# Optimization experiments

Measured on AMD Instinct MI355X. Metric: run time of the kernel, lower is better.

## Reference

```python
import jax, jax.numpy as jnp
import numpy as np

B = 1
N_HEADS = 8
SEQ = 4096
HEAD_DIM = 128
BLOCK = 64          # sparse_block_size == kernel_block_size
LOCAL_BLOCKS = 16
VERT_STRIDE = 8


def _token_mask():
    """Local + vertical-strided block-sparse causal mask, per head.

    Block (qb, kb) is active for head h iff qb >= kb and
    (qb - kb < LOCAL_BLOCKS  or  (kb + h*head_step + 1) % VERT_STRIDE == 0),
    then expanded to token level and AND-ed with the token causal mask.
    """
    nb = SEQ // BLOCK
    qb = jnp.arange(nb)[:, None]                      # [nb, 1]
    kb = jnp.arange(nb)[None, :]                      # [1, nb]
    head_step = max(1, VERT_STRIDE // N_HEADS)        # hetero heads (homo_head=False)
    h = jnp.arange(N_HEADS)[:, None, None]            # [H, 1, 1]
    vert = (kb[None] + h * head_step + 1) % VERT_STRIDE == 0   # [H, 1, nb] -> broadcast
    local = (qb - kb >= 0) & (qb - kb < LOCAL_BLOCKS)          # [nb, nb]
    bmask = (qb >= kb)[None] & (local[None] | vert)            # [H, nb, nb]
    # expand block mask to token level
    tmask = jnp.repeat(jnp.repeat(bmask, BLOCK, axis=1), BLOCK, axis=2)  # [H, S, S]
    causal = jnp.arange(SEQ)[:, None] >= jnp.arange(SEQ)[None, :]
    return tmask & causal[None]


def setup_inputs() -> dict:
    key = jax.random.key(0)
    kq, kk, kv = jax.random.split(key, 3)
    q = jax.random.normal(kq, (B, N_HEADS, SEQ, HEAD_DIM), jnp.float32)
    k = jax.random.normal(kk, (B, N_HEADS, SEQ, HEAD_DIM), jnp.float32)
    v = jax.random.normal(kv, (B, N_HEADS, SEQ, HEAD_DIM), jnp.float32)
    sm_scale = jnp.float32(1.0 / np.sqrt(HEAD_DIM))
    return {"q": q, "k": k, "v": v, "sm_scale": sm_scale}


def reference(q, k, v, sm_scale):
    mask = _token_mask()                                       # [H, S, S] bool
    scores = jnp.einsum('bhqd,bhkd->bhqk', q, k) * sm_scale    # [B, H, S, S]
    neg = jnp.asarray(jnp.finfo(scores.dtype).min, scores.dtype)
    scores = jnp.where(mask[None], scores, neg)
    p = jax.nn.softmax(scores, axis=-1)
    return jnp.einsum('bhqk,bhkd->bhqd', p, v)
```

## Files before the change

kernel.cpp:

```cpp
#include <hip/hip_runtime.h>
#include <hip/hip_bf16.h>

#define HH 8
#define SEQL 4096
#define DD 128
#define NBLK 64
#define LOCAL_B 16
#define MBIAS 12.0f
#define EP_STR 132

typedef __attribute__((ext_vector_type(8))) short bf16x8;
typedef __attribute__((ext_vector_type(4))) float f32x4;
typedef unsigned short ushort_t;

typedef const __attribute__((address_space(1))) unsigned int gu32;
typedef __attribute__((address_space(3))) unsigned int lu32;

__device__ __forceinline__ unsigned short f2bf(float x) {
    union { float f; unsigned u; } a; a.f = x;
    unsigned r = a.u + 0x7FFFu + ((a.u >> 16) & 1u);
    return (unsigned short)(r >> 16);
}

__device__ __forceinline__ unsigned cvtpk_bf16(float lo, float hi) {
    unsigned r;
    asm("v_cvt_pk_bf16_f32 %0, %1, %2" : "=v"(r) : "v"(lo), "v"(hi));
    return r;
}

__device__ __forceinline__ void gload16(const void* src, void* ldsdst) {
    __builtin_amdgcn_global_load_lds((gu32*)src, (lu32*)ldsdst, 16, 0, 0);
}

#define T_STR 136
__global__ void prep(const float* __restrict__ k, const float* __restrict__ v,
                     ushort_t* __restrict__ kb, ushort_t* __restrict__ vt) {
    __shared__ ushort_t t[64 * T_STR];
    int bid = blockIdx.x;
    int tid = threadIdx.x;
    if (bid < 2048) {
        int idx = (bid * 256 + tid) * 8;
        const float4* s = (const float4*)(k + idx);
        float4 a = s[0], b = s[1];
        union { bf16x8 v8; ushort_t u[8]; } p;
        p.u[0] = f2bf(a.x); p.u[1] = f2bf(a.y); p.u[2] = f2bf(a.z); p.u[3] = f2bf(a.w);
        p.u[4] = f2bf(b.x); p.u[5] = f2bf(b.y); p.u[6] = f2bf(b.z); p.u[7] = f2bf(b.w);
        *(bf16x8*)(kb + idx) = p.v8;
        return;
    }
    int g = bid - 2048;
    int h  = g >> 6;
    int sb = g & 63;
    const float* vp = v + ((size_t)h * SEQL + sb * 64) * DD;
    {
        int col = (tid & 15) * 8;
        #pragma unroll
        for (int it = 0; it < 4; ++it) {
            int row = it * 16 + (tid >> 4);
            const float4* s = (const float4*)(vp + row * DD + col);
            float4 a = s[0], b = s[1];
            union { bf16x8 v8; ushort_t u[8]; } p;
            p.u[0] = f2bf(a.x); p.u[1] = f2bf(a.y); p.u[2] = f2bf(a.z); p.u[3] = f2bf(a.w);
            p.u[4] = f2bf(b.x); p.u[5] = f2bf(b.y); p.u[6] = f2bf(b.z); p.u[7] = f2bf(b.w);
            *(bf16x8*)&t[row * T_STR + col] = p.v8;
        }
    }
    __syncthreads();
    {
        int d = tid >> 1, seg = tid & 1;
        ushort_t* dst = vt + ((size_t)h * DD + d) * SEQL + sb * 64 + seg * 32;
        #pragma unroll
        for (int i = 0; i < 4; ++i) {
            union { bf16x8 v8; ushort_t u[8]; } o;
            #pragma unroll
            for (int e = 0; e < 8; ++e)
                o.u[e] = t[(seg * 32 + i * 8 + e) * T_STR + d];
            *(bf16x8*)(dst + i * 8) = o.v8;
        }
    }
}

__global__ __launch_bounds__(256, 2)
void bsattn5(const float* __restrict__ q, const ushort_t* __restrict__ kbuf,
             const ushort_t* __restrict__ vtbuf, const float* __restrict__ scl,
             float* __restrict__ out) {
    const int g  = blockIdx.x;
    const int h  = g & 7;
    const int i0 = g >> 3;
    const int qb = (i0 < 32) ? (63 - i0) : (i0 - 32);
    const int tid = threadIdx.x;
    const int w  = tid >> 6;
    const int l  = tid & 63;
    const int lr = l & 15;
    const int lg = l >> 4;

    __shared__ char smem[65536];

    const float kappa = scl[0] * 1.44269504088896f;

    const float*    qh = q     + (size_t)h * SEQL * DD;
    const ushort_t* kh = kbuf  + (size_t)h * SEQL * DD;
    const ushort_t* vh = vtbuf + (size_t)h * DD * SEQL;
    float*          oh = out   + (size_t)h * SEQL * DD;

    bf16x8 qf[4];
    {
        const float* qrow = qh + (size_t)(qb * 64 + 16 * w + lr) * DD;
        #pragma unroll
        for (int ks = 0; ks < 4; ++ks) {
            const float4* p4 = (const float4*)(qrow + ks * 32 + lg * 8);
            float4 x = p4[0], y = p4[1];
            union { bf16x8 v8; ushort_t u[8]; } pk;
            pk.u[0] = f2bf(x.x * kappa); pk.u[1] = f2bf(x.y * kappa);
            pk.u[2] = f2bf(x.z * kappa); pk.u[3] = f2bf(x.w * kappa);
            pk.u[4] = f2bf(y.x * kappa); pk.u[5] = f2bf(y.y * kappa);
            pk.u[6] = f2bf(y.z * kappa); pk.u[7] = f2bf(y.w * kappa);
            qf[ks] = pk.v8;
        }
    }

    f32x4 oacc[8];
    #pragma unroll
    for (int i = 0; i < 8; ++i) oacc[i] = (f32x4){0.f, 0.f, 0.f, 0.f};
    float lrun = 0.f;

    unsigned swz = (unsigned)((lg * 16) ^ ((lr & 7) << 4));
    unsigned kA = (unsigned)(lr * 256) + swz;
    unsigned kB = kA ^ 64u;
    unsigned vA = 32768u + (unsigned)(lr * 128) + swz;
    unsigned vB = vA ^ 64u;
    unsigned kst = 0, vst = 0;

    auto stage = [&](int kb) {
        const char* kbase = (const char*)(kh + (size_t)kb * 64 * DD);
        char* kdst = smem + kst;
        #pragma unroll
        for (int j = 0; j < 4; ++j) {
            int row  = w * 16 + j * 4 + (l >> 4);
            int colb = ((l & 15) << 4) ^ ((row & 7) << 4);
            gload16(kbase + row * 256 + colb, kdst + (w * 16 + j * 4) * 256);
        }
        const char* vbase = (const char*)vh + (size_t)kb * 128;
        char* vdst = smem + 32768 + vst;
        #pragma unroll
        for (int j = 0; j < 4; ++j) {
            int d0 = w * 32 + j * 8;
            int d  = d0 + (l >> 3);
            int colb = ((l & 7) << 4) ^ ((d & 7) << 4);
            gload16(vbase + (size_t)d * (SEQL * 2) + colb, vdst + d0 * 128);
        }
        kst ^= 16384u; vst ^= 16384u;
    };

    const bool selA = (lg >= 2);
    const bool b1 = (lg & 1);
    const bool b2 = (lg & 2);

    auto compute = [&](bool diag) {
        f32x4 sacc[4];
        #pragma unroll
        for (int ct = 0; ct < 4; ++ct)
            sacc[ct] = (f32x4){-MBIAS, -MBIAS, -MBIAS, -MBIAS};
        __builtin_amdgcn_s_setprio(1);
        #pragma unroll
        for (int ks = 0; ks < 4; ++ks) {
            #pragma unroll
            for (int ct = 0; ct < 4; ++ct) {
                bf16x8 kf = *(const bf16x8*)(smem + ((ks & 1) ? kB : kA) +
                                             ct * 4096 + (ks >> 1) * 128);
                sacc[ct] = __builtin_amdgcn_mfma_f32_16x16x32_bf16(kf, qf[ks], sacc[ct], 0, 0, 0);
            }
        }
        __builtin_amdgcn_s_setprio(0);

        float p[4][4];
        #pragma unroll
        for (int ct = 0; ct < 4; ++ct)
            #pragma unroll
            for (int j = 0; j < 4; ++j)
                p[ct][j] = exp2f(sacc[ct][j]);
        if (diag) {
            #pragma unroll
            for (int ct = 0; ct < 4; ++ct)
                #pragma unroll
                for (int j = 0; j < 4; ++j)
                    if (16 * ct + 4 * lg + j > 16 * w + lr) p[ct][j] = 0.f;
        }
        float rs = 0.f;
        #pragma unroll
        for (int ct = 0; ct < 4; ++ct)
            #pragma unroll
            for (int j = 0; j < 4; ++j) rs += p[ct][j];
        lrun += rs;

        unsigned e0 = cvtpk_bf16(p[0][0], p[0][1]), e1 = cvtpk_bf16(p[0][2], p[0][3]);
        unsigned e2 = cvtpk_bf16(p[2][0], p[2][1]), e3 = cvtpk_bf16(p[2][2], p[2][3]);
        unsigned o0 = cvtpk_bf16(p[1][0], p[1][1]), o1 = cvtpk_bf16(p[1][2], p[1][3]);
        unsigned o2 = cvtpk_bf16(p[3][0], p[3][1]), o3 = cvtpk_bf16(p[3][2], p[3][3]);

        union { unsigned u[4]; bf16x8 v8; } pb0, pb1;
        {
            unsigned m = selA ? o0 : e0, n = selA ? e0 : o0;
            unsigned t  = __shfl_xor((int)n, 32);
            unsigned tp = __shfl_xor((int)n, 48);
            unsigned m16 = __shfl_xor((int)m, 16);
            pb0.u[0] = b1 ? (b2 ? m16 : tp) : (b2 ? t : m);
            pb0.u[2] = b1 ? (b2 ? m : t) : (b2 ? tp : m16);
        }
        {
            unsigned m = selA ? o1 : e1, n = selA ? e1 : o1;
            unsigned t  = __shfl_xor((int)n, 32);
            unsigned tp = __shfl_xor((int)n, 48);
            unsigned m16 = __shfl_xor((int)m, 16);
            pb0.u[1] = b1 ? (b2 ? m16 : tp) : (b2 ? t : m);
            pb0.u[3] = b1 ? (b2 ? m : t) : (b2 ? tp : m16);
        }
        {
            unsigned m = selA ? o2 : e2, n = selA ? e2 : o2;
            unsigned t  = __shfl_xor((int)n, 32);
            unsigned tp = __shfl_xor((int)n, 48);
            unsigned m16 = __shfl_xor((int)m, 16);
            pb1.u[0] = b1 ? (b2 ? m16 : tp) : (b2 ? t : m);
            pb1.u[2] = b1 ? (b2 ? m : t) : (b2 ? tp : m16);
        }
        {
            unsigned m = selA ? o3 : e3, n = selA ? e3 : o3;
            unsigned t  = __shfl_xor((int)n, 32);
            unsigned tp = __shfl_xor((int)n, 48);
            unsigned m16 = __shfl_xor((int)m, 16);
            pb1.u[1] = b1 ? (b2 ? m16 : tp) : (b2 ? t : m);
            pb1.u[3] = b1 ? (b2 ? m : t) : (b2 ? tp : m16);
        }

        __builtin_amdgcn_s_setprio(1);
        #pragma unroll
        for (int dt = 0; dt < 8; ++dt) {
            bf16x8 vf = *(const bf16x8*)(smem + vA + dt * 2048);
            oacc[dt] = __builtin_amdgcn_mfma_f32_16x16x32_bf16(vf, pb0.v8, oacc[dt], 0, 0, 0);
        }
        #pragma unroll
        for (int dt = 0; dt < 8; ++dt) {
            bf16x8 vf = *(const bf16x8*)(smem + vB + dt * 2048);
            oacc[dt] = __builtin_amdgcn_mfma_f32_16x16x32_bf16(vf, pb1.v8, oacc[dt], 0, 0, 0);
        }
        __builtin_amdgcn_s_setprio(0);
    };

    const int vstart = (7 - h) & 7;
    int lo = qb - (LOCAL_B - 1); if (lo < 0) lo = 0;
    int kb = (vstart <= qb - LOCAL_B) ? vstart : lo;
    stage(kb);
    for (;;) {
        int kn;
        if (kb < lo) { int n = kb + 8; kn = (n <= qb - LOCAL_B) ? n : lo; }
        else if (kb < qb) kn = kb + 1;
        else kn = -1;

        if (kn >= 0) {
            stage(kn);
            asm volatile("s_waitcnt vmcnt(8)" ::: "memory");
            __builtin_amdgcn_sched_barrier(0);
            __builtin_amdgcn_s_barrier();
            __builtin_amdgcn_sched_barrier(0);
            compute(false);
            __builtin_amdgcn_s_barrier();
            kA ^= 16384u; kB ^= 16384u; vA ^= 16384u; vB ^= 16384u;
            kb = kn;
        } else {
            asm volatile("s_waitcnt vmcnt(0)" ::: "memory");
            __builtin_amdgcn_sched_barrier(0);
            __builtin_amdgcn_s_barrier();
            __builtin_amdgcn_sched_barrier(0);
            compute(true);
            __builtin_amdgcn_s_barrier();
            break;
        }
    }

    float tot = lrun;
    tot += __shfl_xor(tot, 16);
    tot += __shfl_xor(tot, 32);
    float rcp = 1.0f / tot;

    float* ep  = (float*)smem;
    float* epw = ep + w * 16 * EP_STR;
    #pragma unroll
    for (int dt = 0; dt < 8; ++dt)
        #pragma unroll
        for (int j = 0; j < 4; ++j)
            epw[lr * EP_STR + dt * 16 + 4 * lg + j] = oacc[dt][j] * rcp;
    __syncthreads();
    {
        int qr  = tid >> 2;
        int seg = tid & 3;
        const float* rp = ep + (qr >> 4) * (16 * EP_STR) + (qr & 15) * EP_STR + seg * 32;
        float* op = oh + (size_t)(qb * 64 + qr) * DD + seg * 32;
        #pragma unroll
        for (int i = 0; i < 8; ++i)
            ((float4*)op)[i] = ((const float4*)rp)[i];
    }
}

extern "C" void kernel_launch(void* const* d_in, const int* in_sizes, int n_in,
                              void* d_out, int out_size, void* d_ws, size_t ws_size,
                              hipStream_t stream) {
    const float* q   = (const float*)d_in[0];
    const float* k   = (const float*)d_in[1];
    const float* v   = (const float*)d_in[2];
    const float* scl = (const float*)d_in[3];
    float* out = (float*)d_out;

    ushort_t* Kb = (ushort_t*)d_ws;
    ushort_t* Vt = Kb + (size_t)HH * SEQL * DD;

    prep<<<dim3(2048 + HH * 64), dim3(256), 0, stream>>>(k, v, Kb, Vt);
    bsattn5<<<dim3(HH * NBLK), dim3(256), 0, stream>>>(q, Kb, Vt, scl, out);
}
```

Before: 56.59 us.

## Split KV range of heavy query blocks across two workgroups and merge

Query blocks from index 12 upward now have their key-block list split in half across two workgroups, raising the grid from 512 to 928 workgroups to improve load balance and occupancy. Each workgroup writes unnormalized partial outputs and per-row sums to workspace. A new merge kernel adds the partials and divides by the combined denominator. This relies on the fixed softmax bias (no running max), so the partials add directly. The cost is extra global traffic and a third kernel launch.

```diff
diff --git a/kernel.cpp b/kernel.cpp
--- a/kernel.cpp
+++ b/kernel.cpp
@@ -8,6 +8,9 @@
 #define LOCAL_B 16
 #define MBIAS 12.0f
 #define EP_STR 132
+#define SPLIT_Q0 12
+#define NSPLIT (NBLK - SPLIT_Q0)
+#define UNITS_PER_H (SPLIT_Q0 + NSPLIT*2)
 
 typedef __attribute__((ext_vector_type(8))) short bf16x8;
 typedef __attribute__((ext_vector_type(4))) float f32x4;
@@ -81,13 +84,16 @@
 }
 
 __global__ __launch_bounds__(256, 2)
-void bsattn5(const float* __restrict__ q, const ushort_t* __restrict__ kbuf,
+void bsattn6(const float* __restrict__ q, const ushort_t* __restrict__ kbuf,
              const ushort_t* __restrict__ vtbuf, const float* __restrict__ scl,
-             float* __restrict__ out) {
+             float* __restrict__ out, float* __restrict__ part, float* __restrict__ lws) {
     const int g  = blockIdx.x;
     const int h  = g & 7;
-    const int i0 = g >> 3;
-    const int qb = (i0 < 32) ? (63 - i0) : (i0 - 32);
+    const int u  = g >> 3;
+    int qb, sidx;
+    if (u < 2 * NSPLIT) { qb = NBLK - 1 - (u >> 1); sidx = u & 1; }
+    else { qb = (UNITS_PER_H - 1) - u; sidx = -1; }
+
     const int tid = threadIdx.x;
     const int w  = tid >> 6;
     const int l  = tid & 63;
@@ -102,6 +108,15 @@
     const ushort_t* kh = kbuf  + (size_t)h * SEQL * DD;
     const ushort_t* vh = vtbuf + (size_t)h * DD * SEQL;
     float*          oh = out   + (size_t)h * SEQL * DD;
+
+    const int vstart = (7 - h) & 7;
+    const int lo = (qb >= 15) ? (qb - 15) : 0;
+    const int nl = (qb + 1 < LOCAL_B) ? (qb + 1) : LOCAL_B;
+    const int nv = (qb - LOCAL_B >= vstart) ? ((qb - LOCAL_B - vstart) >> 3) + 1 : 0;
+    const int n  = nv + nl;
+    int t0 = 0, t1 = n;
+    if (sidx == 0) t1 = (n + 1) >> 1;
+    else if (sidx == 1) t0 = (n + 1) >> 1;
 
     bf16x8 qf[4];
     {
@@ -131,6 +146,8 @@
     unsigned vB = vA ^ 64u;
     unsigned kst = 0, vst = 0;
 
+    auto kb_of = [&](int i) { return (i < nv) ? (vstart + 8 * i) : (lo + (i - nv)); };
+
     auto stage = [&](int kb) {
         const char* kbase = (const char*)(kh + (size_t)kb * 64 * DD);
         char* kdst = smem + kst;
@@ -200,33 +217,33 @@
 
         union { unsigned u[4]; bf16x8 v8; } pb0, pb1;
         {
-            unsigned m = selA ? o0 : e0, n = selA ? e0 : o0;
-            unsigned t  = __shfl_xor((int)n, 32);
-            unsigned tp = __shfl_xor((int)n, 48);
+            unsigned m = selA ? o0 : e0, nn = selA ? e0 : o0;
+            unsigned t  = __shfl_xor((int)nn, 32);
+            unsigned tp = __shfl_xor((int)nn, 48);
             unsigned m16 = __shfl_xor((int)m, 16);
             pb0.u[0] = b1 ? (b2 ? m16 : tp) : (b2 ? t : m);
             pb0.u[2] = b1 ? (b2 ? m : t) : (b2 ? tp : m16);
         }
         {
-            unsigned m = selA ? o1 : e1, n = selA ? e1 : o1;
-            unsigned t  = __shfl_xor((int)n, 32);
-            unsigned tp = __shfl_xor((int)n, 48);
+            unsigned m = selA ? o1 : e1, nn = selA ? e1 : o1;
+            unsigned t  = __shfl_xor((int)nn, 32);
+            unsigned tp = __shfl_xor((int)nn, 48);
             unsigned m16 = __shfl_xor((int)m, 16);
             pb0.u[1] = b1 ? (b2 ? m16 : tp) : (b2 ? t : m);
             pb0.u[3] = b1 ? (b2 ? m : t) : (b2 ? tp : m16);
         }
         {
-            unsigned m = selA ? o2 : e2, n = selA ? e2 : o2;
-            unsigned t  = __shfl_xor((int)n, 32);
-            unsigned tp = __shfl_xor((int)n, 48);
+            unsigned m = selA ? o2 : e2, nn = selA ? e2 : o2;
+            unsigned t  = __shfl_xor((int)nn, 32);
+            unsigned tp = __shfl_xor((int)nn, 48);
             unsigned m16 = __shfl_xor((int)m, 16);
             pb1.u[0] = b1 ? (b2 ? m16 : tp) : (b2 ? t : m);
             pb1.u[2] = b1 ? (b2 ? m : t) : (b2 ? tp : m16);
         }
         {
-            unsigned m = selA ? o3 : e3, n = selA ? e3 : o3;
-            unsigned t  = __shfl_xor((int)n, 32);
-            unsigned tp = __shfl_xor((int)n, 48);
+            unsigned m = selA ? o3 : e3, nn = selA ? e3 : o3;
+            unsigned t  = __shfl_xor((int)nn, 32);
+            unsigned tp = __shfl_xor((int)nn, 48);
             unsigned m16 = __shfl_xor((int)m, 16);
             pb1.u[1] = b1 ? (b2 ? m16 : tp) : (b2 ? t : m);
             pb1.u[3] = b1 ? (b2 ? m : t) : (b2 ? tp : m16);
@@ -246,41 +263,29 @@
         __builtin_amdgcn_s_setprio(0);
     };
 
-    const int vstart = (7 - h) & 7;
-    int lo = qb - (LOCAL_B - 1); if (lo < 0) lo = 0;
-    int kb = (vstart <= qb - LOCAL_B) ? vstart : lo;
-    stage(kb);
-    for (;;) {
-        int kn;
-        if (kb < lo) { int n = kb + 8; kn = (n <= qb - LOCAL_B) ? n : lo; }
-        else if (kb < qb) kn = kb + 1;
-        else kn = -1;
-
-        if (kn >= 0) {
-            stage(kn);
+    stage(kb_of(t0));
+    for (int t = t0; t < t1; ++t) {
+        if (t + 1 < t1) {
+            stage(kb_of(t + 1));
             asm volatile("s_waitcnt vmcnt(8)" ::: "memory");
-            __builtin_amdgcn_sched_barrier(0);
-            __builtin_amdgcn_s_barrier();
-            __builtin_amdgcn_sched_barrier(0);
-            compute(false);
-            __builtin_amdgcn_s_barrier();
-            kA ^= 16384u; kB ^= 16384u; vA ^= 16384u; vB ^= 16384u;
-            kb = kn;
         } else {
             asm volatile("s_waitcnt vmcnt(0)" ::: "memory");
-            __builtin_amdgcn_sched_barrier(0);
-            __builtin_amdgcn_s_barrier();
-            __builtin_amdgcn_sched_barrier(0);
-            compute(true);
-            __builtin_amdgcn_s_barrier();
-            break;
-        }
+        }
+        __builtin_amdgcn_sched_barrier(0);
+        __builtin_amdgcn_s_barrier();
+        __builtin_amdgcn_sched_barrier(0);
+        compute(t == n - 1);
+        __builtin_amdgcn_s_barrier();
+        kA ^= 16384u; kB ^= 16384u; vA ^= 16384u; vB ^= 16384u;
     }
 
     float tot = lrun;
     tot += __shfl_xor(tot, 16);
     tot += __shfl_xor(tot, 32);
-    float rcp = 1.0f / tot;
+    {
+        float* ls = lws + ((size_t)(h * 64 + qb) * 2 + (sidx == 1 ? 1 : 0)) * 64;
+        if (lg == 0) ls[w * 16 + lr] = tot;
+    }
 
     float* ep  = (float*)smem;
     float* epw = ep + w * 16 * EP_STR;
@@ -288,16 +293,44 @@
     for (int dt = 0; dt < 8; ++dt)
         #pragma unroll
         for (int j = 0; j < 4; ++j)
-            epw[lr * EP_STR + dt * 16 + 4 * lg + j] = oacc[dt][j] * rcp;
+            epw[lr * EP_STR + dt * 16 + 4 * lg + j] = oacc[dt][j];
     __syncthreads();
     {
+        float* obase = (sidx == 1)
+            ? part + (size_t)(h * NSPLIT + (qb - SPLIT_Q0)) * 8192
+            : oh + (size_t)qb * 64 * DD;
         int qr  = tid >> 2;
         int seg = tid & 3;
         const float* rp = ep + (qr >> 4) * (16 * EP_STR) + (qr & 15) * EP_STR + seg * 32;
-        float* op = oh + (size_t)(qb * 64 + qr) * DD + seg * 32;
+        float* op = obase + (size_t)qr * DD + seg * 32;
         #pragma unroll
         for (int i = 0; i < 8; ++i)
             ((float4*)op)[i] = ((const float4*)rp)[i];
+    }
+}
+
+__global__ void merge(float* __restrict__ out, const float* __restrict__ part,
+                      const float* __restrict__ lws) {
+    int b  = blockIdx.x;
+    int h  = b & 7;
+    int qb = b >> 3;
+    int tid = threadIdx.x;
+    int r = tid >> 2, seg = tid & 3;
+    const float* lrow = lws + (size_t)(h * 64 + qb) * 128;
+    bool sp = (qb >= SPLIT_Q0);
+    float denom = lrow[r] + (sp ? lrow[64 + r] : 0.f);
+    float rcp = 1.0f / denom;
+    float* op = out + ((size_t)h * SEQL + qb * 64 + r) * DD + seg * 32;
+    const float* pp = part + (size_t)(h * NSPLIT + (qb - SPLIT_Q0)) * 8192 + (size_t)r * DD + seg * 32;
+    #pragma unroll
+    for (int i = 0; i < 8; ++i) {
+        float4 a = ((const float4*)op)[i];
+        if (sp) {
+            float4 c = ((const float4*)pp)[i];
+            a.x += c.x; a.y += c.y; a.z += c.z; a.w += c.w;
+        }
+        a.x *= rcp; a.y *= rcp; a.z *= rcp; a.w *= rcp;
+        ((float4*)op)[i] = a;
     }
 }
 
@@ -312,7 +345,10 @@
 
     ushort_t* Kb = (ushort_t*)d_ws;
     ushort_t* Vt = Kb + (size_t)HH * SEQL * DD;
+    float* part  = (float*)(Vt + (size_t)HH * SEQL * DD);
+    float* lws   = part + (size_t)HH * NSPLIT * 8192;
 
     prep<<<dim3(2048 + HH * 64), dim3(256), 0, stream>>>(k, v, Kb, Vt);
-    bsattn5<<<dim3(HH * NBLK), dim3(256), 0, stream>>>(q, Kb, Vt, scl, out);
-}
+    bsattn6<<<dim3(HH * UNITS_PER_H), dim3(256), 0, stream>>>(q, Kb, Vt, scl, out, part, lws);
+    merge<<<dim3(HH * NBLK), dim3(256), 0, stream>>>(out, part, lws);
+}
```

New measurement: 84.09 us. 48.6% more time.

## Split each query block into two 32-row halves with 32-key sub-tiles

Applied to the files above, without the earlier changes.

The attention kernel now launches 1024 workgroups of 128 threads, 2 waves each. Each workgroup handles 32 query rows instead of 64, and each key block is walked as two 32-key sub-tiles. Shared memory is halved to 32 KB and launch bounds allow 4 workgroups per CU. The diagonal handling is reworked so that the first query half stops after the first key sub-tile, which avoids computing fully masked work. The aim is more workgroups and waves to fill the GPU and better load balance across the uneven causal work. The cost is that each K/V tile is loaded separately by the two halves, and the per-step MFMA work is smaller relative to the barriers.

```diff
diff --git a/kernel.cpp b/kernel.cpp
--- a/kernel.cpp
+++ b/kernel.cpp
@@ -80,21 +80,22 @@
     }
 }
 
-__global__ __launch_bounds__(256, 2)
-void bsattn5(const float* __restrict__ q, const ushort_t* __restrict__ kbuf,
+__global__ __launch_bounds__(128, 4)
+void bsattn7(const float* __restrict__ q, const ushort_t* __restrict__ kbuf,
              const ushort_t* __restrict__ vtbuf, const float* __restrict__ scl,
              float* __restrict__ out) {
-    const int g  = blockIdx.x;
-    const int h  = g & 7;
-    const int i0 = g >> 3;
-    const int qb = (i0 < 32) ? (63 - i0) : (i0 - 32);
+    const int g = blockIdx.x;
+    const int h = g & 7;
+    const int u = g >> 3;
+    const int qb   = (u < 64) ? (63 - (u >> 1)) : (31 - ((u - 64) >> 1));
+    const int half = u & 1;
     const int tid = threadIdx.x;
     const int w  = tid >> 6;
     const int l  = tid & 63;
     const int lr = l & 15;
     const int lg = l >> 4;
 
-    __shared__ char smem[65536];
+    __shared__ char smem[32768];
 
     const float kappa = scl[0] * 1.44269504088896f;
 
@@ -105,7 +106,7 @@
 
     bf16x8 qf[4];
     {
-        const float* qrow = qh + (size_t)(qb * 64 + 16 * w + lr) * DD;
+        const float* qrow = qh + (size_t)(qb * 64 + half * 32 + 16 * w + lr) * DD;
         #pragma unroll
         for (int ks = 0; ks < 4; ++ks) {
             const float4* p4 = (const float4*)(qrow + ks * 32 + lg * 8);
@@ -124,32 +125,29 @@
     for (int i = 0; i < 8; ++i) oacc[i] = (f32x4){0.f, 0.f, 0.f, 0.f};
     float lrun = 0.f;
 
-    unsigned swz = (unsigned)((lg * 16) ^ ((lr & 7) << 4));
-    unsigned kA = (unsigned)(lr * 256) + swz;
+    unsigned kA = (unsigned)(lr * 256) + (unsigned)((lg * 16) ^ ((lr & 7) << 4));
     unsigned kB = kA ^ 64u;
-    unsigned vA = 32768u + (unsigned)(lr * 128) + swz;
-    unsigned vB = vA ^ 64u;
+    unsigned vA = 16384u + (unsigned)(lr * 64) + (unsigned)((lg * 16) ^ ((lr & 3) << 4));
     unsigned kst = 0, vst = 0;
 
-    auto stage = [&](int kb) {
-        const char* kbase = (const char*)(kh + (size_t)kb * 64 * DD);
-        char* kdst = smem + kst;
-        #pragma unroll
-        for (int j = 0; j < 4; ++j) {
-            int row  = w * 16 + j * 4 + (l >> 4);
-            int colb = ((l & 15) << 4) ^ ((row & 7) << 4);
-            gload16(kbase + row * 256 + colb, kdst + (w * 16 + j * 4) * 256);
-        }
-        const char* vbase = (const char*)vh + (size_t)kb * 128;
-        char* vdst = smem + 32768 + vst;
-        #pragma unroll
-        for (int j = 0; j < 4; ++j) {
-            int d0 = w * 32 + j * 8;
-            int d  = d0 + (l >> 3);
-            int colb = ((l & 7) << 4) ^ ((d & 7) << 4);
-            gload16(vbase + (size_t)d * (SEQL * 2) + colb, vdst + d0 * 128);
-        }
-        kst ^= 16384u; vst ^= 16384u;
+    auto stage = [&](int s) {
+        const char* kbase = (const char*)kh + (size_t)s * 8192;
+        #pragma unroll
+        for (int i = 0; i < 4; ++i) {
+            int a = i * 2048 + w * 1024 + l * 16;
+            int row = a >> 8, cl = a & 255;
+            gload16(kbase + row * 256 + (cl ^ ((row & 7) << 4)),
+                    smem + kst + i * 2048 + w * 1024);
+        }
+        const char* vbase = (const char*)vh + (size_t)s * 64;
+        #pragma unroll
+        for (int i = 0; i < 4; ++i) {
+            int a = i * 2048 + w * 1024 + l * 16;
+            int d = a >> 6, cl = a & 63;
+            gload16(vbase + (size_t)d * (SEQL * 2) + (cl ^ ((d & 3) << 4)),
+                    smem + 16384 + vst + i * 2048 + w * 1024);
+        }
+        kst ^= 8192u; vst ^= 8192u;
     };
 
     const bool selA = (lg >= 2);
@@ -157,15 +155,15 @@
     const bool b2 = (lg & 2);
 
     auto compute = [&](bool diag) {
-        f32x4 sacc[4];
-        #pragma unroll
-        for (int ct = 0; ct < 4; ++ct)
+        f32x4 sacc[2];
+        #pragma unroll
+        for (int ct = 0; ct < 2; ++ct)
             sacc[ct] = (f32x4){-MBIAS, -MBIAS, -MBIAS, -MBIAS};
         __builtin_amdgcn_s_setprio(1);
         #pragma unroll
         for (int ks = 0; ks < 4; ++ks) {
             #pragma unroll
-            for (int ct = 0; ct < 4; ++ct) {
+            for (int ct = 0; ct < 2; ++ct) {
                 bf16x8 kf = *(const bf16x8*)(smem + ((ks & 1) ? kB : kA) +
                                              ct * 4096 + (ks >> 1) * 128);
                 sacc[ct] = __builtin_amdgcn_mfma_f32_16x16x32_bf16(kf, qf[ks], sacc[ct], 0, 0, 0);
@@ -173,108 +171,90 @@
         }
         __builtin_amdgcn_s_setprio(0);
 
-        float p[4][4];
-        #pragma unroll
-        for (int ct = 0; ct < 4; ++ct)
+        float p[2][4];
+        #pragma unroll
+        for (int ct = 0; ct < 2; ++ct)
             #pragma unroll
             for (int j = 0; j < 4; ++j)
                 p[ct][j] = exp2f(sacc[ct][j]);
         if (diag) {
             #pragma unroll
-            for (int ct = 0; ct < 4; ++ct)
+            for (int ct = 0; ct < 2; ++ct)
                 #pragma unroll
                 for (int j = 0; j < 4; ++j)
                     if (16 * ct + 4 * lg + j > 16 * w + lr) p[ct][j] = 0.f;
         }
         float rs = 0.f;
         #pragma unroll
-        for (int ct = 0; ct < 4; ++ct)
+        for (int ct = 0; ct < 2; ++ct)
             #pragma unroll
             for (int j = 0; j < 4; ++j) rs += p[ct][j];
         lrun += rs;
 
         unsigned e0 = cvtpk_bf16(p[0][0], p[0][1]), e1 = cvtpk_bf16(p[0][2], p[0][3]);
-        unsigned e2 = cvtpk_bf16(p[2][0], p[2][1]), e3 = cvtpk_bf16(p[2][2], p[2][3]);
         unsigned o0 = cvtpk_bf16(p[1][0], p[1][1]), o1 = cvtpk_bf16(p[1][2], p[1][3]);
-        unsigned o2 = cvtpk_bf16(p[3][0], p[3][1]), o3 = cvtpk_bf16(p[3][2], p[3][3]);
-
-        union { unsigned u[4]; bf16x8 v8; } pb0, pb1;
+
+        union { unsigned u[4]; bf16x8 v8; } pb0;
         {
-            unsigned m = selA ? o0 : e0, n = selA ? e0 : o0;
-            unsigned t  = __shfl_xor((int)n, 32);
-            unsigned tp = __shfl_xor((int)n, 48);
+            unsigned m = selA ? o0 : e0, nn = selA ? e0 : o0;
+            unsigned t  = __shfl_xor((int)nn, 32);
+            unsigned tp = __shfl_xor((int)nn, 48);
             unsigned m16 = __shfl_xor((int)m, 16);
             pb0.u[0] = b1 ? (b2 ? m16 : tp) : (b2 ? t : m);
             pb0.u[2] = b1 ? (b2 ? m : t) : (b2 ? tp : m16);
         }
         {
-            unsigned m = selA ? o1 : e1, n = selA ? e1 : o1;
-            unsigned t  = __shfl_xor((int)n, 32);
-            unsigned tp = __shfl_xor((int)n, 48);
+            unsigned m = selA ? o1 : e1, nn = selA ? e1 : o1;
+            unsigned t  = __shfl_xor((int)nn, 32);
+            unsigned tp = __shfl_xor((int)nn, 48);
             unsigned m16 = __shfl_xor((int)m, 16);
             pb0.u[1] = b1 ? (b2 ? m16 : tp) : (b2 ? t : m);
             pb0.u[3] = b1 ? (b2 ? m : t) : (b2 ? tp : m16);
         }
-        {
-            unsigned m = selA ? o2 : e2, n = selA ? e2 : o2;
-            unsigned t  = __shfl_xor((int)n, 32);
-            unsigned tp = __shfl_xor((int)n, 48);
-            unsigned m16 = __shfl_xor((int)m, 16);
-            pb1.u[0] = b1 ? (b2 ? m16 : tp) : (b2 ? t : m);
-            pb1.u[2] = b1 ? (b2 ? m : t) : (b2 ? tp : m16);
-        }
-        {
-            unsigned m = selA ? o3 : e3, n = selA ? e3 : o3;
-            unsigned t  = __shfl_xor((int)n, 32);
-            unsigned tp = __shfl_xor((int)n, 48);
-            unsigned m16 = __shfl_xor((int)m, 16);
-            pb1.u[1] = b1 ? (b2 ? m16 : tp) : (b2 ? t : m);
-            pb1.u[3] = b1 ? (b2 ? m : t) : (b2 ? tp : m16);
-        }
 
         __builtin_amdgcn_s_setprio(1);
         #pragma unroll
         for (int dt = 0; dt < 8; ++dt) {
-            bf16x8 vf = *(const bf16x8*)(smem + vA + dt * 2048);
+            bf16x8 vf = *(const bf16x8*)(smem + vA + dt * 1024);
             oacc[dt] = __builtin_amdgcn_mfma_f32_16x16x32_bf16(vf, pb0.v8, oacc[dt], 0, 0, 0);
-        }
-        #pragma unroll
-        for (int dt = 0; dt < 8; ++dt) {
-            bf16x8 vf = *(const bf16x8*)(smem + vB + dt * 2048);
-            oacc[dt] = __builtin_amdgcn_mfma_f32_16x16x32_bf16(vf, pb1.v8, oacc[dt], 0, 0, 0);
         }
         __builtin_amdgcn_s_setprio(0);
     };
 
     const int vstart = (7 - h) & 7;
-    int lo = qb - (LOCAL_B - 1); if (lo < 0) lo = 0;
+    const int lo = (qb >= 15) ? (qb - 15) : 0;
     int kb = (vstart <= qb - LOCAL_B) ? vstart : lo;
-    stage(kb);
+    int ph = 0;
+    stage(kb * 2);
     for (;;) {
-        int kn;
-        if (kb < lo) { int n = kb + 8; kn = (n <= qb - LOCAL_B) ? n : lo; }
-        else if (kb < qb) kn = kb + 1;
-        else kn = -1;
-
-        if (kn >= 0) {
-            stage(kn);
+        const bool masked = (kb == qb) && (!half || ph == 1);
+        bool last;
+        int nkb = kb, nph = 0;
+        if (ph == 0) {
+            if (kb == qb && half == 0) last = true;
+            else { nph = 1; last = false; }
+        } else {
+            if (kb == qb) last = true;
+            else {
+                nkb = (kb < lo) ? ((kb + 8 <= qb - LOCAL_B) ? kb + 8 : lo) : (kb + 1);
+                last = false;
+            }
+        }
+
+        if (!last) {
+            stage(nkb * 2 + nph);
             asm volatile("s_waitcnt vmcnt(8)" ::: "memory");
-            __builtin_amdgcn_sched_barrier(0);
-            __builtin_amdgcn_s_barrier();
-            __builtin_amdgcn_sched_barrier(0);
-            compute(false);
-            __builtin_amdgcn_s_barrier();
-            kA ^= 16384u; kB ^= 16384u; vA ^= 16384u; vB ^= 16384u;
-            kb = kn;
         } else {
             asm volatile("s_waitcnt vmcnt(0)" ::: "memory");
-            __builtin_amdgcn_sched_barrier(0);
-            __builtin_amdgcn_s_barrier();
-            __builtin_amdgcn_sched_barrier(0);
-            compute(true);
-            __builtin_amdgcn_s_barrier();
-            break;
-        }
+        }
+        __builtin_amdgcn_sched_barrier(0);
+        __builtin_amdgcn_s_barrier();
+        __builtin_amdgcn_sched_barrier(0);
+        compute(masked);
+        __builtin_amdgcn_s_barrier();
+        kA ^= 8192u; kB ^= 8192u; vA ^= 8192u;
+        if (last) break;
+        kb = nkb; ph = nph;
     }
 
     float tot = lrun;
@@ -294,7 +274,7 @@
         int qr  = tid >> 2;
         int seg = tid & 3;
         const float* rp = ep + (qr >> 4) * (16 * EP_STR) + (qr & 15) * EP_STR + seg * 32;
-        float* op = oh + (size_t)(qb * 64 + qr) * DD + seg * 32;
+        float* op = oh + (size_t)(qb * 64 + half * 32 + qr) * DD + seg * 32;
         #pragma unroll
         for (int i = 0; i < 8; ++i)
             ((float4*)op)[i] = ((const float4*)rp)[i];
@@ -314,5 +294,5 @@
     ushort_t* Vt = Kb + (size_t)HH * SEQL * DD;
 
     prep<<<dim3(2048 + HH * 64), dim3(256), 0, stream>>>(k, v, Kb, Vt);
-    bsattn5<<<dim3(HH * NBLK), dim3(256), 0, stream>>>(q, Kb, Vt, scl, out);
-}
+    bsattn7<<<dim3(HH * 128), dim3(128), 0, stream>>>(q, Kb, Vt, scl, out);
+}
```

After: 69.97 us. 1.24x slower.

## Process two query blocks per workgroup to share K/V staging

Applied to the files above, without the earlier changes.

The attention kernel now launches 512-thread workgroups, each covering two adjacent 64-row query blocks, so every staged K/V tile in shared memory feeds eight waves instead of four. The kernel walks the union of both query blocks' active key blocks. A per-wave activity flag zeroes probabilities for blocks that do not apply to that wave's query block, and the diagonal mask uses the wave's index within its half. This roughly halves global and LDS-staging traffic per output row and halves the number of workgroups. The cost is some wasted MFMA work on inactive tiles (the extra local block at the boundary), a larger shared-memory footprint, and one big workgroup per CU in place of two smaller ones.

```diff
diff --git a/kernel.cpp b/kernel.cpp
--- a/kernel.cpp
+++ b/kernel.cpp
@@ -80,21 +80,23 @@
     }
 }
 
-__global__ __launch_bounds__(256, 2)
-void bsattn5(const float* __restrict__ q, const ushort_t* __restrict__ kbuf,
-             const ushort_t* __restrict__ vtbuf, const float* __restrict__ scl,
-             float* __restrict__ out) {
-    const int g  = blockIdx.x;
-    const int h  = g & 7;
-    const int i0 = g >> 3;
-    const int qb = (i0 < 32) ? (63 - i0) : (i0 - 32);
+__global__ __launch_bounds__(512, 2)
+void bsattn11(const float* __restrict__ q, const ushort_t* __restrict__ kbuf,
+              const ushort_t* __restrict__ vtbuf, const float* __restrict__ scl,
+              float* __restrict__ out) {
+    const int g = blockIdx.x;
+    const int h = g & 7;
+    const int p = 31 - (g >> 3);
+    const int qmax = 2 * p + 1;
     const int tid = threadIdx.x;
     const int w  = tid >> 6;
+    const int half = w >> 2;
+    const int qtok = 2 * p + half;
     const int l  = tid & 63;
     const int lr = l & 15;
     const int lg = l >> 4;
 
-    __shared__ char smem[65536];
+    __shared__ char smem[69632];
 
     const float kappa = scl[0] * 1.44269504088896f;
 
@@ -105,7 +107,7 @@
 
     bf16x8 qf[4];
     {
-        const float* qrow = qh + (size_t)(qb * 64 + 16 * w + lr) * DD;
+        const float* qrow = qh + (size_t)(p * 128 + 16 * w + lr) * DD;
         #pragma unroll
         for (int ks = 0; ks < 4; ++ks) {
             const float4* p4 = (const float4*)(qrow + ks * 32 + lg * 8);
@@ -124,30 +126,28 @@
     for (int i = 0; i < 8; ++i) oacc[i] = (f32x4){0.f, 0.f, 0.f, 0.f};
     float lrun = 0.f;
 
-    unsigned swz = (unsigned)((lg * 16) ^ ((lr & 7) << 4));
-    unsigned kA = (unsigned)(lr * 256) + swz;
+    unsigned kA = (unsigned)(lr * 256) + (unsigned)((lg * 16) ^ ((lr & 7) << 4));
     unsigned kB = kA ^ 64u;
-    unsigned vA = 32768u + (unsigned)(lr * 128) + swz;
+    unsigned vA = 32768u + (unsigned)(lr * 128) + (unsigned)((lg * 16) ^ ((lr & 7) << 4));
     unsigned vB = vA ^ 64u;
     unsigned kst = 0, vst = 0;
 
     auto stage = [&](int kb) {
         const char* kbase = (const char*)(kh + (size_t)kb * 64 * DD);
-        char* kdst = smem + kst;
-        #pragma unroll
-        for (int j = 0; j < 4; ++j) {
-            int row  = w * 16 + j * 4 + (l >> 4);
-            int colb = ((l & 15) << 4) ^ ((row & 7) << 4);
-            gload16(kbase + row * 256 + colb, kdst + (w * 16 + j * 4) * 256);
+        #pragma unroll
+        for (int i = 0; i < 2; ++i) {
+            int row = w * 8 + i * 4 + (l >> 4);
+            int col = (l & 15) * 16;
+            gload16(kbase + row * 256 + (col ^ ((row & 7) << 4)),
+                    smem + kst + (w * 8 + i * 4) * 256);
         }
         const char* vbase = (const char*)vh + (size_t)kb * 128;
-        char* vdst = smem + 32768 + vst;
-        #pragma unroll
-        for (int j = 0; j < 4; ++j) {
-            int d0 = w * 32 + j * 8;
-            int d  = d0 + (l >> 3);
-            int colb = ((l & 7) << 4) ^ ((d & 7) << 4);
-            gload16(vbase + (size_t)d * (SEQL * 2) + colb, vdst + d0 * 128);
+        #pragma unroll
+        for (int i = 0; i < 2; ++i) {
+            int d = w * 16 + i * 8 + (l >> 3);
+            int c = (l & 7) * 16;
+            gload16(vbase + (size_t)d * (SEQL * 2) + (c ^ ((d & 7) << 4)),
+                    smem + 32768 + vst + (w * 16 + i * 8) * 128);
         }
         kst ^= 16384u; vst ^= 16384u;
     };
@@ -155,8 +155,9 @@
     const bool selA = (lg >= 2);
     const bool b1 = (lg & 1);
     const bool b2 = (lg & 2);
-
-    auto compute = [&](bool diag) {
+    const int vstart = (7 - h) & 7;
+
+    auto compute = [&](bool act, bool dg) {
         f32x4 sacc[4];
         #pragma unroll
         for (int ct = 0; ct < 4; ++ct)
@@ -173,60 +174,65 @@
         }
         __builtin_amdgcn_s_setprio(0);
 
-        float p[4][4];
+        float pv[4][4];
         #pragma unroll
         for (int ct = 0; ct < 4; ++ct)
             #pragma unroll
             for (int j = 0; j < 4; ++j)
-                p[ct][j] = exp2f(sacc[ct][j]);
-        if (diag) {
+                pv[ct][j] = exp2f(sacc[ct][j]);
+        if (!act) {
+            #pragma unroll
+            for (int ct = 0; ct < 4; ++ct)
+                #pragma unroll
+                for (int j = 0; j < 4; ++j) pv[ct][j] = 0.f;
+        } else if (dg) {
             #pragma unroll
             for (int ct = 0; ct < 4; ++ct)
                 #pragma unroll
                 for (int j = 0; j < 4; ++j)
-                    if (16 * ct + 4 * lg + j > 16 * w + lr) p[ct][j] = 0.f;
+                    if (16 * ct + 4 * lg + j > 16 * (w & 3) + lr) pv[ct][j] = 0.f;
         }
         float rs = 0.f;
         #pragma unroll
         for (int ct = 0; ct < 4; ++ct)
             #pragma unroll
-            for (int j = 0; j < 4; ++j) rs += p[ct][j];
+            for (int j = 0; j < 4; ++j) rs += pv[ct][j];
         lrun += rs;
 
-        unsigned e0 = cvtpk_bf16(p[0][0], p[0][1]), e1 = cvtpk_bf16(p[0][2], p[0][3]);
-        unsigned e2 = cvtpk_bf16(p[2][0], p[2][1]), e3 = cvtpk_bf16(p[2][2], p[2][3]);
-        unsigned o0 = cvtpk_bf16(p[1][0], p[1][1]), o1 = cvtpk_bf16(p[1][2], p[1][3]);
-        unsigned o2 = cvtpk_bf16(p[3][0], p[3][1]), o3 = cvtpk_bf16(p[3][2], p[3][3]);
+        unsigned e0 = cvtpk_bf16(pv[0][0], pv[0][1]), e1 = cvtpk_bf16(pv[0][2], pv[0][3]);
+        unsigned e2 = cvtpk_bf16(pv[2][0], pv[2][1]), e3 = cvtpk_bf16(pv[2][2], pv[2][3]);
+        unsigned o0 = cvtpk_bf16(pv[1][0], pv[1][1]), o1 = cvtpk_bf16(pv[1][2], pv[1][3]);
+        unsigned o2 = cvtpk_bf16(pv[3][0], pv[3][1]), o3 = cvtpk_bf16(pv[3][2], pv[3][3]);
 
         union { unsigned u[4]; bf16x8 v8; } pb0, pb1;
         {
-            unsigned m = selA ? o0 : e0, n = selA ? e0 : o0;
-            unsigned t  = __shfl_xor((int)n, 32);
-            unsigned tp = __shfl_xor((int)n, 48);
+            unsigned m = selA ? o0 : e0, nn = selA ? e0 : o0;
+            unsigned t  = __shfl_xor((int)nn, 32);
+            unsigned tp = __shfl_xor((int)nn, 48);
             unsigned m16 = __shfl_xor((int)m, 16);
             pb0.u[0] = b1 ? (b2 ? m16 : tp) : (b2 ? t : m);
             pb0.u[2] = b1 ? (b2 ? m : t) : (b2 ? tp : m16);
         }
         {
-            unsigned m = selA ? o1 : e1, n = selA ? e1 : o1;
-            unsigned t  = __shfl_xor((int)n, 32);
-            unsigned tp = __shfl_xor((int)n, 48);
+            unsigned m = selA ? o1 : e1, nn = selA ? e1 : o1;
+            unsigned t  = __shfl_xor((int)nn, 32);
+            unsigned tp = __shfl_xor((int)nn, 48);
             unsigned m16 = __shfl_xor((int)m, 16);
             pb0.u[1] = b1 ? (b2 ? m16 : tp) : (b2 ? t : m);
             pb0.u[3] = b1 ? (b2 ? m : t) : (b2 ? tp : m16);
         }
         {
-            unsigned m = selA ? o2 : e2, n = selA ? e2 : o2;
-            unsigned t  = __shfl_xor((int)n, 32);
-            unsigned tp = __shfl_xor((int)n, 48);
+            unsigned m = selA ? o2 : e2, nn = selA ? e2 : o2;
+            unsigned t  = __shfl_xor((int)nn, 32);
+            unsigned tp = __shfl_xor((int)nn, 48);
             unsigned m16 = __shfl_xor((int)m, 16);
             pb1.u[0] = b1 ? (b2 ? m16 : tp) : (b2 ? t : m);
             pb1.u[2] = b1 ? (b2 ? m : t) : (b2 ? tp : m16);
         }
         {
-            unsigned m = selA ? o3 : e3, n = selA ? e3 : o3;
-            unsigned t  = __shfl_xor((int)n, 32);
-            unsigned tp = __shfl_xor((int)n, 48);
+            unsigned m = selA ? o3 : e3, nn = selA ? e3 : o3;
+            unsigned t  = __shfl_xor((int)nn, 32);
+            unsigned tp = __shfl_xor((int)nn, 48);
             unsigned m16 = __shfl_xor((int)m, 16);
             pb1.u[1] = b1 ? (b2 ? m16 : tp) : (b2 ? t : m);
             pb1.u[3] = b1 ? (b2 ? m : t) : (b2 ? tp : m16);
@@ -246,35 +252,34 @@
         __builtin_amdgcn_s_setprio(0);
     };
 
-    const int vstart = (7 - h) & 7;
-    int lo = qb - (LOCAL_B - 1); if (lo < 0) lo = 0;
-    int kb = (vstart <= qb - LOCAL_B) ? vstart : lo;
+    const int lo  = (2 * p - 15 > 0) ? (2 * p - 15) : 0;
+    const int vend = 2 * p - 16;
+    int kb = (lo > 0 && vstart <= vend) ? vstart : lo;
     stage(kb);
     for (;;) {
         int kn;
-        if (kb < lo) { int n = kb + 8; kn = (n <= qb - LOCAL_B) ? n : lo; }
-        else if (kb < qb) kn = kb + 1;
+        if (kb < lo) { int n = kb + 8; kn = (n <= vend) ? n : lo; }
+        else if (kb < qmax) kn = kb + 1;
         else kn = -1;
 
         if (kn >= 0) {
             stage(kn);
-            asm volatile("s_waitcnt vmcnt(8)" ::: "memory");
-            __builtin_amdgcn_sched_barrier(0);
-            __builtin_amdgcn_s_barrier();
-            __builtin_amdgcn_sched_barrier(0);
-            compute(false);
-            __builtin_amdgcn_s_barrier();
-            kA ^= 16384u; kB ^= 16384u; vA ^= 16384u; vB ^= 16384u;
-            kb = kn;
+            asm volatile("s_waitcnt vmcnt(4)" ::: "memory");
         } else {
             asm volatile("s_waitcnt vmcnt(0)" ::: "memory");
-            __builtin_amdgcn_sched_barrier(0);
-            __builtin_amdgcn_s_barrier();
-            __builtin_amdgcn_sched_barrier(0);
-            compute(true);
-            __builtin_amdgcn_s_barrier();
-            break;
-        }
+        }
+        __builtin_amdgcn_sched_barrier(0);
+        __builtin_amdgcn_s_barrier();
+        __builtin_amdgcn_sched_barrier(0);
+
+        bool act = (kb <= qtok) && ((qtok - kb < LOCAL_B) || ((kb & 7) == vstart));
+        bool dg  = (kb == qtok);
+        compute(act, dg);
+
+        __builtin_amdgcn_s_barrier();
+        kA ^= 16384u; kB ^= 16384u; vA ^= 16384u; vB ^= 16384u;
+        if (kn < 0) break;
+        kb = kn;
     }
 
     float tot = lrun;
@@ -294,7 +299,7 @@
         int qr  = tid >> 2;
         int seg = tid & 3;
         const float* rp = ep + (qr >> 4) * (16 * EP_STR) + (qr & 15) * EP_STR + seg * 32;
-        float* op = oh + (size_t)(qb * 64 + qr) * DD + seg * 32;
+        float* op = oh + (size_t)(p * 128 + qr) * DD + seg * 32;
         #pragma unroll
         for (int i = 0; i < 8; ++i)
             ((float4*)op)[i] = ((const float4*)rp)[i];
@@ -314,5 +319,5 @@
     ushort_t* Vt = Kb + (size_t)HH * SEQL * DD;
 
     prep<<<dim3(2048 + HH * 64), dim3(256), 0, stream>>>(k, v, Kb, Vt);
-    bsattn5<<<dim3(HH * NBLK), dim3(256), 0, stream>>>(q, Kb, Vt, scl, out);
-}
+    bsattn11<<<dim3(HH * 32), dim3(512), 0, stream>>>(q, Kb, Vt, scl, out);
+}
```

Result: slower. 68.08 us (+20.3%).
